# Optimization experiments

Hardware: AMD Instinct MI355X
Metric: run time of the kernel (lower is better)

The kernel has to match this reference:

```python
import jax, jax.numpy as jnp
import numpy as np

D_MODEL = 1024
N_HEADS = 16
D_K = D_MODEL // N_HEADS


def setup_inputs() -> dict:
    key = jax.random.key(0)
    ks = jax.random.split(key, 9)
    s = 1.0 / np.sqrt(D_MODEL)
    inp = {
        "x": jax.random.normal(ks[0], (4, 2048, D_MODEL), dtype=jnp.float32),
        "wq": jax.random.normal(ks[1], (D_MODEL, D_MODEL), dtype=jnp.float32) * s,
        "bq": jax.random.normal(ks[2], (D_MODEL,), dtype=jnp.float32) * 0.01,
        "wk": jax.random.normal(ks[3], (D_MODEL, D_MODEL), dtype=jnp.float32) * s,
        "bk": jax.random.normal(ks[4], (D_MODEL,), dtype=jnp.float32) * 0.01,
        "wv": jax.random.normal(ks[5], (D_MODEL, D_MODEL), dtype=jnp.float32) * s,
        "bv": jax.random.normal(ks[6], (D_MODEL,), dtype=jnp.float32) * 0.01,
        "wo": jax.random.normal(ks[7], (D_MODEL, D_MODEL), dtype=jnp.float32) * s,
        "bo": jax.random.normal(ks[8], (D_MODEL,), dtype=jnp.float32) * 0.01,
    }
    return inp


def reference(x, wq, bq, wk, bk, wv, bv, wo, bo):
    B, S, _ = x.shape
    # QKV projections (weights stored [in, out] so y = x @ w + b)
    q = (x @ wq + bq).reshape(B, S, N_HEADS, D_K).transpose(0, 2, 1, 3)  # [B,H,S,Dk]
    k = (x @ wk + bk).reshape(B, S, N_HEADS, D_K).transpose(0, 2, 1, 3)
    v = (x @ wv + bv).reshape(B, S, N_HEADS, D_K).transpose(0, 2, 1, 3)
    scale = 1.0 / jnp.sqrt(jnp.asarray(D_K, dtype=x.dtype))
    scores = jnp.einsum("bhqd,bhkd->bhqk", q, k) * scale  # [B,H,S,S]
    attn = jax.nn.softmax(scores, axis=-1)
    out = jnp.einsum("bhqk,bhkd->bhqd", attn, v)  # [B,H,S,Dk]
    out = out.transpose(0, 2, 1, 3).reshape(B, S, D_MODEL)
    return out @ wo + bo
```

## Files before the change

kernel.cpp:

```cpp
#include <hip/hip_runtime.h>

#define D_MODEL 1024
#define NH 16
#define DK 64
#define BB 4
#define SS 2048
#define MROWS (BB*SS)

typedef __attribute__((ext_vector_type(4))) float f32x4;
typedef __attribute__((ext_vector_type(16))) float f32x16;
typedef __attribute__((ext_vector_type(8))) short short8;
typedef __attribute__((ext_vector_type(4))) float float4v;
typedef __attribute__((ext_vector_type(2))) unsigned u32x2;

typedef const __attribute__((address_space(1))) void* gas_t;
typedef __attribute__((address_space(3))) void* las_t;

static __device__ __forceinline__ ushort f2bf(float f) {
  union { float f; unsigned u; } v; v.f = f;
  unsigned r = 0x7fffu + ((v.u >> 16) & 1u);
  return (ushort)((v.u + r) >> 16);
}

__global__ __launch_bounds__(256) void convert_x_k(const float* __restrict__ x,
                                                   ushort* __restrict__ xb) {
  int i = blockIdx.x * 256 + threadIdx.x;
  float4v v = ((const float4v*)x)[i];
  ushort4 o;
  o.x = f2bf(v.x); o.y = f2bf(v.y); o.z = f2bf(v.z); o.w = f2bf(v.w);
  ((ushort4*)xb)[i] = o;
}

__global__ __launch_bounds__(256) void convert_wt_k(const float* __restrict__ w,
                                                    ushort* __restrict__ wt) {
  __shared__ float tile[64][65];
  int bx = blockIdx.x, by = blockIdx.y;
  int tx = threadIdx.x & 63, ty = threadIdx.x >> 6;
#pragma unroll
  for (int i = 0; i < 16; ++i) {
    int r = i * 4 + ty;
    tile[r][tx] = w[(size_t)(by * 64 + r) * D_MODEL + bx * 64 + tx];
  }
  __syncthreads();
#pragma unroll
  for (int i = 0; i < 16; ++i) {
    int r = i * 4 + ty;
    wt[(size_t)(bx * 64 + r) * D_MODEL + by * 64 + tx] = f2bf(tile[tx][r]);
  }
}

template <int MODE>
__global__ __launch_bounds__(256) void gemm_bt_k(const ushort* __restrict__ A,
                                                 const ushort* __restrict__ Bt,
                                                 const float* __restrict__ bias,
                                                 void* __restrict__ outp,
                                                 float scale) {
  const int M = MROWS, N = D_MODEL, K = D_MODEL;
  __shared__ __align__(16) ushort As[128 * 32];
  __shared__ __align__(16) ushort Bs[128 * 32];
  const int nbn = N / 128;
  const int nwg = (M / 128) * nbn;
  int bid = blockIdx.x;
  int wg = (bid & 7) * (nwg >> 3) + (bid >> 3);
  int bm = wg / nbn, bn = wg % nbn;
  const int t = threadIdx.x;
  const int l = t & 63;
  const int w = t >> 6;
  const int g = l >> 4, q = l & 15;
  const int wr = w >> 1, wc = w & 1;

  f32x4 acc[4][4];
#pragma unroll
  for (int m = 0; m < 4; ++m)
#pragma unroll
    for (int n = 0; n < 4; ++n) acc[m][n] = f32x4{0.f, 0.f, 0.f, 0.f};

  const ushort* Ab = A + (size_t)bm * 128 * K;
  const ushort* Bb = Bt + (size_t)bn * 128 * K;

  for (int kt = 0; kt < K; kt += 32) {
    __syncthreads();
#pragma unroll
    for (int i = 0; i < 2; ++i) {
      int c = i * 256 + t;
      __builtin_amdgcn_global_load_lds((gas_t)(Ab + (size_t)(c >> 2) * K + kt + (c & 3) * 8),
                                       (las_t)(As + c * 8), 16, 0, 0);
      __builtin_amdgcn_global_load_lds((gas_t)(Bb + (size_t)(c >> 2) * K + kt + (c & 3) * 8),
                                       (las_t)(Bs + c * 8), 16, 0, 0);
    }
    __syncthreads();
    short8 af[4], bf[4];
#pragma unroll
    for (int m = 0; m < 4; ++m)
      af[m] = *(const short8*)(As + (wr * 64 + m * 16 + q) * 32 + g * 8);
#pragma unroll
    for (int n = 0; n < 4; ++n)
      bf[n] = *(const short8*)(Bs + (wc * 64 + n * 16 + q) * 32 + g * 8);
#pragma unroll
    for (int m = 0; m < 4; ++m)
#pragma unroll
      for (int n = 0; n < 4; ++n)
        acc[m][n] = __builtin_amdgcn_mfma_f32_16x16x32_bf16(af[m], bf[n], acc[m][n], 0, 0, 0);
  }

  const int rbase0 = bm * 128 + wr * 64 + g * 4;
  const int cbase = bn * 128 + wc * 64 + q;
#pragma unroll
  for (int m = 0; m < 4; ++m) {
    int r0 = rbase0 + m * 16;
#pragma unroll
    for (int n = 0; n < 4; ++n) {
      int c = cbase + n * 16;
      float bv = bias[c];
      if (MODE == 1) {
        ushort4 pk;
        pk.x = f2bf((acc[m][n][0] + bv) * scale);
        pk.y = f2bf((acc[m][n][1] + bv) * scale);
        pk.z = f2bf((acc[m][n][2] + bv) * scale);
        pk.w = f2bf((acc[m][n][3] + bv) * scale);
        size_t off = (((size_t)((r0 >> 11) * NH + (c >> 6))) * DK + (c & 63)) * (size_t)SS + (r0 & (SS - 1));
        *(ushort4*)((ushort*)outp + off) = pk;
      } else {
#pragma unroll
        for (int j = 0; j < 4; ++j) {
          int r = r0 + j;
          float v = (acc[m][n][j] + bv) * scale;
          if (MODE == 0) {
            size_t off = (((size_t)((r >> 11) * NH + (c >> 6))) * SS + (r & (SS - 1))) * DK + (c & 63);
            ((ushort*)outp)[off] = f2bf(v);
          } else {
            ((float*)outp)[(size_t)r * D_MODEL + c] = v;
          }
        }
      }
    }
  }
}

__global__ __launch_bounds__(256, 2) void attn_k(const ushort* __restrict__ Qm,
                                                 const ushort* __restrict__ Km,
                                                 const ushort* __restrict__ Vm,
                                                 ushort* __restrict__ Ob) {
  __shared__ __align__(16) ushort Ks[2][64 * 64];
  __shared__ __align__(16) ushort Vs[2][64 * 64];
  const int bid = blockIdx.x;
  const int logical = (bid & 7) * 64 + (bid >> 3);
  const int bh = logical >> 3;
  const int qblk = logical & 7;
  const int t = threadIdx.x, l = t & 63, w = t >> 6;
  const int q = l & 31, h = l >> 5;
  const int qsw = q & 7;

  const ushort* Qb = Qm + ((size_t)bh * SS + qblk * 256 + w * 64) * DK;
  const ushort* Kb = Km + (size_t)bh * SS * DK;
  const ushort* Vb = Vm + (size_t)bh * DK * SS;

  short8 qf[2][4];
#pragma unroll
  for (int qg = 0; qg < 2; ++qg)
#pragma unroll
    for (int ks = 0; ks < 4; ++ks)
      qf[qg][ks] = *(const short8*)(Qb + (qg * 32 + q) * DK + ks * 16 + h * 8);

  f32x16 oacc[2][2];
#pragma unroll
  for (int qg = 0; qg < 2; ++qg)
#pragma unroll
    for (int d = 0; d < 2; ++d)
#pragma unroll
      for (int r = 0; r < 16; ++r) oacc[qg][d][r] = 0.f;
  float lrun[2] = {0.f, 0.f};

  const int cg = (l & 7) ^ ((l >> 3) & 7);

#define STAGE(B, KT)                                                                        \
  do {                                                                                      \
    _Pragma("unroll") for (int i_ = 0; i_ < 2; ++i_) {                                      \
      int row_ = w * 16 + i_ * 8 + (l >> 3);                                                \
      __builtin_amdgcn_global_load_lds((gas_t)(Kb + (size_t)((KT) + row_) * DK + cg * 8),   \
                                       (las_t)(Ks[B] + (w * 16 + i_ * 8) * 64 + l * 8),     \
                                       16, 0, 0);                                           \
      __builtin_amdgcn_global_load_lds((gas_t)(Vb + (size_t)row_ * SS + (KT) + cg * 8),     \
                                       (las_t)(Vs[B] + (w * 16 + i_ * 8) * 64 + l * 8),     \
                                       16, 0, 0);                                           \
    }                                                                                       \
  } while (0)

  STAGE(0, 0);
  int cur = 0;

  for (int kt = 0; kt < SS; kt += 64) {
    __syncthreads();
    if (kt + 64 < SS) STAGE(cur ^ 1, kt + 64);

    f32x16 sc[2][2];
#pragma unroll
    for (int qg = 0; qg < 2; ++qg)
#pragma unroll
      for (int n = 0; n < 2; ++n)
#pragma unroll
        for (int r = 0; r < 16; ++r) sc[qg][n][r] = 0.f;

    __builtin_amdgcn_s_setprio(1);
#pragma unroll
    for (int ks = 0; ks < 4; ++ks)
#pragma unroll
      for (int n = 0; n < 2; ++n) {
        short8 kf = *(const short8*)(Ks[cur] + (n * 32 + q) * 64 + ((ks * 2 + h) ^ qsw) * 8);
        sc[0][n] = __builtin_amdgcn_mfma_f32_32x32x16_bf16(kf, qf[0][ks], sc[0][n], 0, 0, 0);
        sc[1][n] = __builtin_amdgcn_mfma_f32_32x32x16_bf16(kf, qf[1][ks], sc[1][n], 0, 0, 0);
      }
    __builtin_amdgcn_s_setprio(0);

    short8 pf[2][4];
#pragma unroll
    for (int qg = 0; qg < 2; ++qg) {
#pragma unroll
      for (int n = 0; n < 2; ++n)
#pragma unroll
        for (int r = 0; r < 16; ++r) sc[qg][n][r] = __builtin_amdgcn_exp2f(sc[qg][n][r]);

      float s8[8];
#pragma unroll
      for (int i = 0; i < 8; ++i)
        s8[i] = (sc[qg][0][i] + sc[qg][0][i + 8]) + (sc[qg][1][i] + sc[qg][1][i + 8]);
#pragma unroll
      for (int i = 0; i < 4; ++i) s8[i] += s8[i + 4];
      lrun[qg] += (s8[0] + s8[1]) + (s8[2] + s8[3]);

#pragma unroll
      for (int n = 0; n < 2; ++n) {
        unsigned wv[8];
#pragma unroll
        for (int Qd = 0; Qd < 4; ++Qd) {
          unsigned w0, w1;
          asm("v_cvt_pk_bf16_f32 %0, %1, %2" : "=v"(w0) : "v"(sc[qg][n][Qd * 4 + 0]), "v"(sc[qg][n][Qd * 4 + 1]));
          asm("v_cvt_pk_bf16_f32 %0, %1, %2" : "=v"(w1) : "v"(sc[qg][n][Qd * 4 + 2]), "v"(sc[qg][n][Qd * 4 + 3]));
          wv[Qd * 2] = w0; wv[Qd * 2 + 1] = w1;
        }
#pragma unroll
        for (int m = 0; m < 2; ++m) {
          u32x2 r0 = __builtin_amdgcn_permlane32_swap(wv[(2 * m) * 2 + 0], wv[(2 * m + 1) * 2 + 0], false, false);
          u32x2 r1 = __builtin_amdgcn_permlane32_swap(wv[(2 * m) * 2 + 1], wv[(2 * m + 1) * 2 + 1], false, false);
          union { unsigned u[4]; short8 s; } fu;
          fu.u[0] = r0[0]; fu.u[1] = r1[0]; fu.u[2] = r0[1]; fu.u[3] = r1[1];
          pf[qg][n * 2 + m] = fu.s;
        }
      }
    }

    __builtin_amdgcn_s_setprio(1);
#pragma unroll
    for (int kvb = 0; kvb < 4; ++kvb)
#pragma unroll
      for (int d = 0; d < 2; ++d) {
        short8 vf = *(const short8*)(Vs[cur] + (d * 32 + q) * 64 + ((kvb * 2 + h) ^ qsw) * 8);
        oacc[0][d] = __builtin_amdgcn_mfma_f32_32x32x16_bf16(vf, pf[0][kvb], oacc[0][d], 0, 0, 0);
        oacc[1][d] = __builtin_amdgcn_mfma_f32_32x32x16_bf16(vf, pf[1][kvb], oacc[1][d], 0, 0, 0);
      }
    __builtin_amdgcn_s_setprio(0);
    cur ^= 1;
  }
#undef STAGE

  const int b_ = bh >> 4, h_ = bh & 15;
#pragma unroll
  for (int qg = 0; qg < 2; ++qg) {
    float lt = lrun[qg];
    lt += __shfl_xor(lt, 32);
    float inv = 1.0f / lt;
    const int srow = qblk * 256 + w * 64 + qg * 32 + q;
#pragma unroll
    for (int d = 0; d < 2; ++d)
#pragma unroll
      for (int rq = 0; rq < 4; ++rq) {
        ushort4 pk;
        pk.x = f2bf(oacc[qg][d][rq * 4 + 0] * inv);
        pk.y = f2bf(oacc[qg][d][rq * 4 + 1] * inv);
        pk.z = f2bf(oacc[qg][d][rq * 4 + 2] * inv);
        pk.w = f2bf(oacc[qg][d][rq * 4 + 3] * inv);
        size_t off = ((size_t)b_ * SS + srow) * D_MODEL + h_ * 64 + d * 32 + rq * 8 + h * 4;
        *(ushort4*)(Ob + off) = pk;
      }
  }
}

extern "C" void kernel_launch(void* const* d_in, const int* in_sizes, int n_in,
                              void* d_out, int out_size, void* d_ws, size_t ws_size,
                              hipStream_t stream) {
  (void)in_sizes; (void)n_in; (void)out_size; (void)ws_size;
  const float* x  = (const float*)d_in[0];
  const float* wq = (const float*)d_in[1];
  const float* bq = (const float*)d_in[2];
  const float* wk = (const float*)d_in[3];
  const float* bk = (const float*)d_in[4];
  const float* wv = (const float*)d_in[5];
  const float* bv = (const float*)d_in[6];
  const float* wo = (const float*)d_in[7];
  const float* bo = (const float*)d_in[8];

  char* ws = (char*)d_ws;
  ushort* xb  = (ushort*)(ws);
  ushort* wqt = (ushort*)(ws + 16777216);
  ushort* wkt = (ushort*)(ws + 16777216 + 1 * 2097152);
  ushort* wvt = (ushort*)(ws + 16777216 + 2 * 2097152);
  ushort* wot = (ushort*)(ws + 16777216 + 3 * 2097152);
  ushort* Qw  = (ushort*)(ws + 16777216 + 4 * 2097152);
  ushort* Kw  = (ushort*)(ws + 16777216 + 4 * 2097152 + 16777216);
  ushort* Vw  = (ushort*)(ws + 16777216 + 4 * 2097152 + 2 * 16777216);
  ushort* Obw = xb;

  convert_x_k<<<MROWS * D_MODEL / 4 / 256, 256, 0, stream>>>(x, xb);
  convert_wt_k<<<dim3(16, 16), 256, 0, stream>>>(wq, wqt);
  convert_wt_k<<<dim3(16, 16), 256, 0, stream>>>(wk, wkt);
  convert_wt_k<<<dim3(16, 16), 256, 0, stream>>>(wv, wvt);
  convert_wt_k<<<dim3(16, 16), 256, 0, stream>>>(wo, wot);

  gemm_bt_k<0><<<512, 256, 0, stream>>>(xb, wqt, bq, (void*)Qw, 0.125f * 1.44269504088896f);
  gemm_bt_k<0><<<512, 256, 0, stream>>>(xb, wkt, bk, (void*)Kw, 1.0f);
  gemm_bt_k<1><<<512, 256, 0, stream>>>(xb, wvt, bv, (void*)Vw, 1.0f);

  attn_k<<<512, 256, 0, stream>>>(Qw, Kw, Vw, Obw);

  gemm_bt_k<2><<<512, 256, 0, stream>>>(Obw, wot, bo, d_out, 1.0f);
}
```

Measured before the change: 201.7 us.

## Fuse QKV projections into one GEMM and interleave attention softmax with PV MFMAs

Concatenates the transposed Q, K and V weights so a single 1536-block GEMM computes all three projections, choosing bias, scale and output layout per column section in the epilogue. This removes two kernel launches and their tail effects. In the attention loop, K and V fragments are preloaded into registers and the two query groups are processed separately, so one group's exp/pack can overlap the other's MFMAs. The cost is higher register pressure and more epilogue branching.

```diff
diff --git a/kernel.cpp b/kernel.cpp
--- a/kernel.cpp
+++ b/kernel.cpp
@@ -49,19 +49,21 @@
   }
 }
 
-template <int MODE>
-__global__ __launch_bounds__(256) void gemm_bt_k(const ushort* __restrict__ A,
-                                                 const ushort* __restrict__ Bt,
-                                                 const float* __restrict__ bias,
-                                                 void* __restrict__ outp,
-                                                 float scale) {
-  const int M = MROWS, N = D_MODEL, K = D_MODEL;
+__global__ __launch_bounds__(256) void gemm_qkv_k(const ushort* __restrict__ A,
+                                                  const ushort* __restrict__ Bt,
+                                                  const float* __restrict__ bq,
+                                                  const float* __restrict__ bk,
+                                                  const float* __restrict__ bv,
+                                                  ushort* __restrict__ Qw,
+                                                  ushort* __restrict__ Kw,
+                                                  ushort* __restrict__ Vw,
+                                                  float qscale) {
+  const int K = D_MODEL;
   __shared__ __align__(16) ushort As[128 * 32];
   __shared__ __align__(16) ushort Bs[128 * 32];
-  const int nbn = N / 128;
-  const int nwg = (M / 128) * nbn;
+  const int nbn = 24;
   int bid = blockIdx.x;
-  int wg = (bid & 7) * (nwg >> 3) + (bid >> 3);
+  int wg = (bid & 7) * 192 + (bid >> 3);
   int bm = wg / nbn, bn = wg % nbn;
   const int t = threadIdx.x;
   const int l = t & 63;
@@ -103,6 +105,91 @@
         acc[m][n] = __builtin_amdgcn_mfma_f32_16x16x32_bf16(af[m], bf[n], acc[m][n], 0, 0, 0);
   }
 
+  const int sec = (bn * 128) >> 10;
+  const float* bias = sec == 0 ? bq : (sec == 1 ? bk : bv);
+  const float scale = sec == 0 ? qscale : 1.0f;
+  ushort* dst = sec == 0 ? Qw : Kw;
+  const int rbase0 = bm * 128 + wr * 64 + g * 4;
+  const int cbase = (bn * 128 + wc * 64 + q) & 1023;
+#pragma unroll
+  for (int m = 0; m < 4; ++m) {
+    int r0 = rbase0 + m * 16;
+#pragma unroll
+    for (int n = 0; n < 4; ++n) {
+      int c = cbase + n * 16;
+      float bv_ = bias[c];
+      if (sec == 2) {
+        ushort4 pk;
+        pk.x = f2bf(acc[m][n][0] + bv_);
+        pk.y = f2bf(acc[m][n][1] + bv_);
+        pk.z = f2bf(acc[m][n][2] + bv_);
+        pk.w = f2bf(acc[m][n][3] + bv_);
+        size_t off = (((size_t)((r0 >> 11) * NH + (c >> 6))) * DK + (c & 63)) * (size_t)SS + (r0 & (SS - 1));
+        *(ushort4*)(Vw + off) = pk;
+      } else {
+#pragma unroll
+        for (int j = 0; j < 4; ++j) {
+          int r = r0 + j;
+          float v = (acc[m][n][j] + bv_) * scale;
+          size_t off = (((size_t)((r >> 11) * NH + (c >> 6))) * SS + (r & (SS - 1))) * DK + (c & 63);
+          dst[off] = f2bf(v);
+        }
+      }
+    }
+  }
+}
+
+__global__ __launch_bounds__(256) void gemm_out_k(const ushort* __restrict__ A,
+                                                  const ushort* __restrict__ Bt,
+                                                  const float* __restrict__ bias,
+                                                  float* __restrict__ outp) {
+  const int K = D_MODEL;
+  __shared__ __align__(16) ushort As[128 * 32];
+  __shared__ __align__(16) ushort Bs[128 * 32];
+  const int nbn = 8;
+  int bid = blockIdx.x;
+  int wg = (bid & 7) * 64 + (bid >> 3);
+  int bm = wg / nbn, bn = wg % nbn;
+  const int t = threadIdx.x;
+  const int l = t & 63;
+  const int w = t >> 6;
+  const int g = l >> 4, q = l & 15;
+  const int wr = w >> 1, wc = w & 1;
+
+  f32x4 acc[4][4];
+#pragma unroll
+  for (int m = 0; m < 4; ++m)
+#pragma unroll
+    for (int n = 0; n < 4; ++n) acc[m][n] = f32x4{0.f, 0.f, 0.f, 0.f};
+
+  const ushort* Ab = A + (size_t)bm * 128 * K;
+  const ushort* Bb = Bt + (size_t)bn * 128 * K;
+
+  for (int kt = 0; kt < K; kt += 32) {
+    __syncthreads();
+#pragma unroll
+    for (int i = 0; i < 2; ++i) {
+      int c = i * 256 + t;
+      __builtin_amdgcn_global_load_lds((gas_t)(Ab + (size_t)(c >> 2) * K + kt + (c & 3) * 8),
+                                       (las_t)(As + c * 8), 16, 0, 0);
+      __builtin_amdgcn_global_load_lds((gas_t)(Bb + (size_t)(c >> 2) * K + kt + (c & 3) * 8),
+                                       (las_t)(Bs + c * 8), 16, 0, 0);
+    }
+    __syncthreads();
+    short8 af[4], bf[4];
+#pragma unroll
+    for (int m = 0; m < 4; ++m)
+      af[m] = *(const short8*)(As + (wr * 64 + m * 16 + q) * 32 + g * 8);
+#pragma unroll
+    for (int n = 0; n < 4; ++n)
+      bf[n] = *(const short8*)(Bs + (wc * 64 + n * 16 + q) * 32 + g * 8);
+#pragma unroll
+    for (int m = 0; m < 4; ++m)
+#pragma unroll
+      for (int n = 0; n < 4; ++n)
+        acc[m][n] = __builtin_amdgcn_mfma_f32_16x16x32_bf16(af[m], bf[n], acc[m][n], 0, 0, 0);
+  }
+
   const int rbase0 = bm * 128 + wr * 64 + g * 4;
   const int cbase = bn * 128 + wc * 64 + q;
 #pragma unroll
@@ -112,27 +199,9 @@
     for (int n = 0; n < 4; ++n) {
       int c = cbase + n * 16;
       float bv = bias[c];
-      if (MODE == 1) {
-        ushort4 pk;
-        pk.x = f2bf((acc[m][n][0] + bv) * scale);
-        pk.y = f2bf((acc[m][n][1] + bv) * scale);
-        pk.z = f2bf((acc[m][n][2] + bv) * scale);
-        pk.w = f2bf((acc[m][n][3] + bv) * scale);
-        size_t off = (((size_t)((r0 >> 11) * NH + (c >> 6))) * DK + (c & 63)) * (size_t)SS + (r0 & (SS - 1));
-        *(ushort4*)((ushort*)outp + off) = pk;
-      } else {
-#pragma unroll
-        for (int j = 0; j < 4; ++j) {
-          int r = r0 + j;
-          float v = (acc[m][n][j] + bv) * scale;
-          if (MODE == 0) {
-            size_t off = (((size_t)((r >> 11) * NH + (c >> 6))) * SS + (r & (SS - 1))) * DK + (c & 63);
-            ((ushort*)outp)[off] = f2bf(v);
-          } else {
-            ((float*)outp)[(size_t)r * D_MODEL + c] = v;
-          }
-        }
-      }
+#pragma unroll
+      for (int j = 0; j < 4; ++j)
+        outp[(size_t)(r0 + j) * D_MODEL + c] = acc[m][n][j] + bv;
     }
   }
 }
@@ -162,13 +231,15 @@
     for (int ks = 0; ks < 4; ++ks)
       qf[qg][ks] = *(const short8*)(Qb + (qg * 32 + q) * DK + ks * 16 + h * 8);
 
+  f32x16 zf;
+#pragma unroll
+  for (int r = 0; r < 16; ++r) zf[r] = 0.f;
+
   f32x16 oacc[2][2];
 #pragma unroll
   for (int qg = 0; qg < 2; ++qg)
 #pragma unroll
-    for (int d = 0; d < 2; ++d)
-#pragma unroll
-      for (int r = 0; r < 16; ++r) oacc[qg][d][r] = 0.f;
+    for (int d = 0; d < 2; ++d) oacc[qg][d] = zf;
   float lrun[2] = {0.f, 0.f};
 
   const int cg = (l & 7) ^ ((l >> 3) & 7);
@@ -186,6 +257,38 @@
     }                                                                                       \
   } while (0)
 
+#define SOFTMAX_PACK(QG, SC, PF)                                                            \
+  do {                                                                                      \
+    _Pragma("unroll") for (int n = 0; n < 2; ++n)                                           \
+      _Pragma("unroll") for (int r = 0; r < 16; ++r)                                        \
+        SC[n][r] = __builtin_amdgcn_exp2f(SC[n][r]);                                        \
+    float s8[8];                                                                            \
+    _Pragma("unroll") for (int i = 0; i < 8; ++i)                                           \
+      s8[i] = (SC[0][i] + SC[0][i + 8]) + (SC[1][i] + SC[1][i + 8]);                        \
+    _Pragma("unroll") for (int i = 0; i < 4; ++i) s8[i] += s8[i + 4];                       \
+    lrun[QG] += (s8[0] + s8[1]) + (s8[2] + s8[3]);                                          \
+    _Pragma("unroll") for (int n = 0; n < 2; ++n) {                                         \
+      unsigned wv[8];                                                                       \
+      _Pragma("unroll") for (int Qd = 0; Qd < 4; ++Qd) {                                    \
+        unsigned w0, w1;                                                                    \
+        asm("v_cvt_pk_bf16_f32 %0, %1, %2" : "=v"(w0)                                       \
+            : "v"(SC[n][Qd * 4 + 0]), "v"(SC[n][Qd * 4 + 1]));                              \
+        asm("v_cvt_pk_bf16_f32 %0, %1, %2" : "=v"(w1)                                       \
+            : "v"(SC[n][Qd * 4 + 2]), "v"(SC[n][Qd * 4 + 3]));                              \
+        wv[Qd * 2] = w0; wv[Qd * 2 + 1] = w1;                                               \
+      }                                                                                     \
+      _Pragma("unroll") for (int m = 0; m < 2; ++m) {                                       \
+        u32x2 r0 = __builtin_amdgcn_permlane32_swap(wv[(2 * m) * 2 + 0],                    \
+                                                    wv[(2 * m + 1) * 2 + 0], false, false); \
+        u32x2 r1 = __builtin_amdgcn_permlane32_swap(wv[(2 * m) * 2 + 1],                    \
+                                                    wv[(2 * m + 1) * 2 + 1], false, false); \
+        union { unsigned u[4]; short8 s; } fu;                                              \
+        fu.u[0] = r0[0]; fu.u[1] = r1[0]; fu.u[2] = r0[1]; fu.u[3] = r1[1];                 \
+        PF[n * 2 + m] = fu.s;                                                               \
+      }                                                                                     \
+    }                                                                                       \
+  } while (0)
+
   STAGE(0, 0);
   int cur = 0;
 
@@ -193,75 +296,69 @@
     __syncthreads();
     if (kt + 64 < SS) STAGE(cur ^ 1, kt + 64);
 
-    f32x16 sc[2][2];
-#pragma unroll
-    for (int qg = 0; qg < 2; ++qg)
+    const ushort* Kc = Ks[cur];
+    const ushort* Vc = Vs[cur];
+
+    short8 kf[2][4];
+#pragma unroll
+    for (int ks = 0; ks < 4; ++ks) {
+      int ch = ((ks * 2 + h) ^ qsw) * 8;
 #pragma unroll
       for (int n = 0; n < 2; ++n)
-#pragma unroll
-        for (int r = 0; r < 16; ++r) sc[qg][n][r] = 0.f;
-
+        kf[n][ks] = *(const short8*)(Kc + (n * 32 + q) * 64 + ch);
+    }
+
+    f32x16 sc0[2], sc1[2];
     __builtin_amdgcn_s_setprio(1);
 #pragma unroll
-    for (int ks = 0; ks < 4; ++ks)
-#pragma unroll
-      for (int n = 0; n < 2; ++n) {
-        short8 kf = *(const short8*)(Ks[cur] + (n * 32 + q) * 64 + ((ks * 2 + h) ^ qsw) * 8);
-        sc[0][n] = __builtin_amdgcn_mfma_f32_32x32x16_bf16(kf, qf[0][ks], sc[0][n], 0, 0, 0);
-        sc[1][n] = __builtin_amdgcn_mfma_f32_32x32x16_bf16(kf, qf[1][ks], sc[1][n], 0, 0, 0);
-      }
+    for (int n = 0; n < 2; ++n)
+      sc0[n] = __builtin_amdgcn_mfma_f32_32x32x16_bf16(kf[n][0], qf[0][0], zf, 0, 0, 0);
+#pragma unroll
+    for (int ks = 1; ks < 4; ++ks)
+#pragma unroll
+      for (int n = 0; n < 2; ++n)
+        sc0[n] = __builtin_amdgcn_mfma_f32_32x32x16_bf16(kf[n][ks], qf[0][ks], sc0[n], 0, 0, 0);
+#pragma unroll
+    for (int n = 0; n < 2; ++n)
+      sc1[n] = __builtin_amdgcn_mfma_f32_32x32x16_bf16(kf[n][0], qf[1][0], zf, 0, 0, 0);
+#pragma unroll
+    for (int ks = 1; ks < 4; ++ks)
+#pragma unroll
+      for (int n = 0; n < 2; ++n)
+        sc1[n] = __builtin_amdgcn_mfma_f32_32x32x16_bf16(kf[n][ks], qf[1][ks], sc1[n], 0, 0, 0);
     __builtin_amdgcn_s_setprio(0);
 
-    short8 pf[2][4];
-#pragma unroll
-    for (int qg = 0; qg < 2; ++qg) {
-#pragma unroll
-      for (int n = 0; n < 2; ++n)
-#pragma unroll
-        for (int r = 0; r < 16; ++r) sc[qg][n][r] = __builtin_amdgcn_exp2f(sc[qg][n][r]);
-
-      float s8[8];
-#pragma unroll
-      for (int i = 0; i < 8; ++i)
-        s8[i] = (sc[qg][0][i] + sc[qg][0][i + 8]) + (sc[qg][1][i] + sc[qg][1][i + 8]);
-#pragma unroll
-      for (int i = 0; i < 4; ++i) s8[i] += s8[i + 4];
-      lrun[qg] += (s8[0] + s8[1]) + (s8[2] + s8[3]);
-
-#pragma unroll
-      for (int n = 0; n < 2; ++n) {
-        unsigned wv[8];
-#pragma unroll
-        for (int Qd = 0; Qd < 4; ++Qd) {
-          unsigned w0, w1;
-          asm("v_cvt_pk_bf16_f32 %0, %1, %2" : "=v"(w0) : "v"(sc[qg][n][Qd * 4 + 0]), "v"(sc[qg][n][Qd * 4 + 1]));
-          asm("v_cvt_pk_bf16_f32 %0, %1, %2" : "=v"(w1) : "v"(sc[qg][n][Qd * 4 + 2]), "v"(sc[qg][n][Qd * 4 + 3]));
-          wv[Qd * 2] = w0; wv[Qd * 2 + 1] = w1;
-        }
-#pragma unroll
-        for (int m = 0; m < 2; ++m) {
-          u32x2 r0 = __builtin_amdgcn_permlane32_swap(wv[(2 * m) * 2 + 0], wv[(2 * m + 1) * 2 + 0], false, false);
-          u32x2 r1 = __builtin_amdgcn_permlane32_swap(wv[(2 * m) * 2 + 1], wv[(2 * m + 1) * 2 + 1], false, false);
-          union { unsigned u[4]; short8 s; } fu;
-          fu.u[0] = r0[0]; fu.u[1] = r1[0]; fu.u[2] = r0[1]; fu.u[3] = r1[1];
-          pf[qg][n * 2 + m] = fu.s;
-        }
-      }
-    }
-
+    short8 vf[2][4];
+#pragma unroll
+    for (int kvb = 0; kvb < 4; ++kvb) {
+      int ch = ((kvb * 2 + h) ^ qsw) * 8;
+#pragma unroll
+      for (int d = 0; d < 2; ++d)
+        vf[d][kvb] = *(const short8*)(Vc + (d * 32 + q) * 64 + ch);
+    }
+
+    short8 pf0[4], pf1[4];
+    SOFTMAX_PACK(0, sc0, pf0);
     __builtin_amdgcn_s_setprio(1);
 #pragma unroll
     for (int kvb = 0; kvb < 4; ++kvb)
 #pragma unroll
-      for (int d = 0; d < 2; ++d) {
-        short8 vf = *(const short8*)(Vs[cur] + (d * 32 + q) * 64 + ((kvb * 2 + h) ^ qsw) * 8);
-        oacc[0][d] = __builtin_amdgcn_mfma_f32_32x32x16_bf16(vf, pf[0][kvb], oacc[0][d], 0, 0, 0);
-        oacc[1][d] = __builtin_amdgcn_mfma_f32_32x32x16_bf16(vf, pf[1][kvb], oacc[1][d], 0, 0, 0);
-      }
+      for (int d = 0; d < 2; ++d)
+        oacc[0][d] = __builtin_amdgcn_mfma_f32_32x32x16_bf16(vf[d][kvb], pf0[kvb], oacc[0][d], 0, 0, 0);
+    __builtin_amdgcn_s_setprio(0);
+
+    SOFTMAX_PACK(1, sc1, pf1);
+    __builtin_amdgcn_s_setprio(1);
+#pragma unroll
+    for (int kvb = 0; kvb < 4; ++kvb)
+#pragma unroll
+      for (int d = 0; d < 2; ++d)
+        oacc[1][d] = __builtin_amdgcn_mfma_f32_32x32x16_bf16(vf[d][kvb], pf1[kvb], oacc[1][d], 0, 0, 0);
     __builtin_amdgcn_s_setprio(0);
     cur ^= 1;
   }
 #undef STAGE
+#undef SOFTMAX_PACK
 
   const int b_ = bh >> 4, h_ = bh & 15;
 #pragma unroll
@@ -300,27 +397,24 @@
   const float* bo = (const float*)d_in[8];
 
   char* ws = (char*)d_ws;
-  ushort* xb  = (ushort*)(ws);
-  ushort* wqt = (ushort*)(ws + 16777216);
-  ushort* wkt = (ushort*)(ws + 16777216 + 1 * 2097152);
-  ushort* wvt = (ushort*)(ws + 16777216 + 2 * 2097152);
-  ushort* wot = (ushort*)(ws + 16777216 + 3 * 2097152);
-  ushort* Qw  = (ushort*)(ws + 16777216 + 4 * 2097152);
-  ushort* Kw  = (ushort*)(ws + 16777216 + 4 * 2097152 + 16777216);
-  ushort* Vw  = (ushort*)(ws + 16777216 + 4 * 2097152 + 2 * 16777216);
-  ushort* Obw = xb;
+  ushort* xb    = (ushort*)(ws);
+  ushort* wqkvt = (ushort*)(ws + 16777216);
+  ushort* wot   = (ushort*)(ws + 16777216 + 6291456);
+  ushort* Qw    = (ushort*)(ws + 16777216 + 6291456 + 2097152);
+  ushort* Kw    = (ushort*)(ws + 16777216 + 6291456 + 2097152 + 16777216);
+  ushort* Vw    = (ushort*)(ws + 16777216 + 6291456 + 2097152 + 2 * 16777216);
+  ushort* Obw   = xb;
 
   convert_x_k<<<MROWS * D_MODEL / 4 / 256, 256, 0, stream>>>(x, xb);
-  convert_wt_k<<<dim3(16, 16), 256, 0, stream>>>(wq, wqt);
-  convert_wt_k<<<dim3(16, 16), 256, 0, stream>>>(wk, wkt);
-  convert_wt_k<<<dim3(16, 16), 256, 0, stream>>>(wv, wvt);
+  convert_wt_k<<<dim3(16, 16), 256, 0, stream>>>(wq, wqkvt);
+  convert_wt_k<<<dim3(16, 16), 256, 0, stream>>>(wk, wqkvt + 1024 * 1024);
+  convert_wt_k<<<dim3(16, 16), 256, 0, stream>>>(wv, wqkvt + 2 * 1024 * 1024);
   convert_wt_k<<<dim3(16, 16), 256, 0, stream>>>(wo, wot);
 
-  gemm_bt_k<0><<<512, 256, 0, stream>>>(xb, wqt, bq, (void*)Qw, 0.125f * 1.44269504088896f);
-  gemm_bt_k<0><<<512, 256, 0, stream>>>(xb, wkt, bk, (void*)Kw, 1.0f);
-  gemm_bt_k<1><<<512, 256, 0, stream>>>(xb, wvt, bv, (void*)Vw, 1.0f);
+  gemm_qkv_k<<<1536, 256, 0, stream>>>(xb, wqkvt, bq, bk, bv, Qw, Kw, Vw,
+                                       0.125f * 1.44269504088896f);
 
   attn_k<<<512, 256, 0, stream>>>(Qw, Kw, Vw, Obw);
 
-  gemm_bt_k<2><<<512, 256, 0, stream>>>(Obw, wot, bo, d_out, 1.0f);
-}
+  gemm_out_k<<<512, 256, 0, stream>>>(Obw, wot, bo, (float*)d_out);
+}
```

After: 201.8 us. No clear change (+0.1%).
